# Kernel tuning notes

Hardware: AMD Instinct MI355X
Metric: run time of the kernel (lower is better)

## Reference

```python
import jax, jax.numpy as jnp
import numpy as np

DG = 8   # deformable_groups
KK = 9   # 3x3 kernel
NEG_SLOPE = 0.2


def conv3x3(x, w, b):
    y = jax.lax.conv_general_dilated(x, w, (1, 1), ((1, 1), (1, 1)),
                                     dimension_numbers=('NCHW', 'OIHW', 'NCHW'))
    return y + b[None, :, None, None]


def deform_sample(x, oy, ox, mask):
    # x: [B,C,H,W]; oy/ox/mask: [B,DG,KK,H,W] -> sampled [B,DG,cpg,KK,H,W]
    B, C, H, W = x.shape
    cpg = C // DG
    ky, kx = jnp.meshgrid(jnp.arange(3), jnp.arange(3), indexing='ij')
    ky = (ky.reshape(-1) - 1).astype(x.dtype)  # dilation=1, padding=1
    kx = (kx.reshape(-1) - 1).astype(x.dtype)
    hh = jnp.arange(H, dtype=x.dtype)
    ww = jnp.arange(W, dtype=x.dtype)
    py = hh[None, None, None, :, None] + ky[None, None, :, None, None] + oy
    px = ww[None, None, None, None, :] + kx[None, None, :, None, None] + ox
    y0 = jnp.floor(py)
    x0 = jnp.floor(px)
    fy = py - y0
    fx = px - x0
    xg = x.reshape(B, DG, cpg, H * W)

    def gather(yi, xi):
        valid = ((yi >= 0) & (yi < H) & (xi >= 0) & (xi < W)).astype(x.dtype)
        yc = jnp.clip(yi, 0, H - 1)
        xc = jnp.clip(xi, 0, W - 1)
        idx = (yc * W + xc).reshape(B, DG, 1, KK * H * W)
        v = jnp.take_along_axis(xg, idx, axis=3).reshape(B, DG, cpg, KK, H, W)
        return v * valid[:, :, None]

    y0i = y0.astype(jnp.int32)
    x0i = x0.astype(jnp.int32)
    v00 = gather(y0i, x0i)
    v01 = gather(y0i, x0i + 1)
    v10 = gather(y0i + 1, x0i)
    v11 = gather(y0i + 1, x0i + 1)
    wy = fy[:, :, None]
    wx = fx[:, :, None]
    val = (v00 * (1 - wy) * (1 - wx) + v01 * (1 - wy) * wx
           + v10 * wy * (1 - wx) + v11 * wy * wx)
    return val * mask[:, :, None]


def reference(x, offset, w_off, b_off, w_dcn, b_dcn, w_conv1, b_conv1):
    B, C, H, W = x.shape
    om = conv3x3(offset, w_off, b_off)  # [B, 3*DG*KK, H, W]
    o1, o2, m = jnp.split(om, 3, axis=1)
    oy = o1.reshape(B, DG, KK, H, W)
    ox = o2.reshape(B, DG, KK, H, W)
    mask = jax.nn.sigmoid(m).reshape(B, DG, KK, H, W)
    sampled = deform_sample(x, oy, ox, mask)  # [B,DG,cpg,KK,H,W]
    wd = w_dcn.reshape(w_dcn.shape[0], DG, C // DG, KK)
    dcn = jnp.einsum('bgckhw,ogck->bohw', sampled, wd) + b_dcn[None, :, None, None]
    fea = jnp.where(dcn >= 0, dcn, NEG_SLOPE * dcn)  # LeakyReLU(0.2)
    out = conv3x3(fea, w_conv1, b_conv1) + x  # residual
    return out


def setup_inputs() -> dict:
    key = jax.random.key(0)
    ks = jax.random.split(key, 8)
    B, C, H, W = 4, 64, 96, 96
    offC = 64
    s = 1.0 / np.sqrt(C * 9)
    return {
        'x': jax.random.normal(ks[0], (B, C, H, W), jnp.float32),
        'offset': jax.random.normal(ks[1], (B, offC, H, W), jnp.float32),
        'w_off': jax.random.normal(ks[2], (3 * DG * KK, offC, 3, 3), jnp.float32) * 0.05,
        'b_off': jnp.zeros((3 * DG * KK,), jnp.float32),
        'w_dcn': jax.random.normal(ks[3], (C, C, 3, 3), jnp.float32) * s,
        'b_dcn': jnp.zeros((C,), jnp.float32),
        'w_conv1': jax.random.normal(ks[4], (C, C, 3, 3), jnp.float32) * s,
        'b_conv1': jnp.zeros((C,), jnp.float32),
    }
```

## Files before the change

kernel.cpp:

```cpp
#include <hip/hip_runtime.h>
#include <math.h>

#define HH 96
#define WW 96
#define NB 4
#define NC 64
#define HW (HH*WW)
#define PH 98
#define PW 98
#define PHW (PH*PW)
#define NPP (NB*PHW)

typedef unsigned short u16;
typedef unsigned int   u32;
typedef __attribute__((ext_vector_type(8))) short bf16x8;
typedef __attribute__((ext_vector_type(4))) float f32x4;

__device__ inline float bf2f(u16 v) { u32 u = ((u32)v) << 16; return __uint_as_float(u); }
__device__ inline u16 f2bf(float f) {
    u32 u = __float_as_uint(f);
    return (u16)((u + 0x7FFFu + ((u >> 16) & 1u)) >> 16);
}
__device__ __forceinline__ float elemf(const u32* a, int i) {
    u32 v = a[i >> 1];
    v = (i & 1) ? (v & 0xFFFF0000u) : (v << 16);
    return __uint_as_float(v);
}

__global__ __launch_bounds__(256) void k_prep(
    const float* __restrict__ x, const float* __restrict__ offset,
    const float* __restrict__ w_off, const float* __restrict__ w_dcn,
    const float* __restrict__ w_c1,
    u16* __restrict__ xt, u16* __restrict__ otp,
    u16* __restrict__ d_off, u16* __restrict__ d_dcn, u16* __restrict__ d_c1) {
    int bx = blockIdx.x;
    int tid = threadIdx.x;
    if (bx < 144) {
        int pix = bx * 256 + tid;
        int b = pix / HW, hw = pix % HW;
        const float* s = x + b * 64 * HW + hw;
        uint4* dp = (uint4*)(xt + pix * 64);
#pragma unroll
        for (int q = 0; q < 8; ++q) {
            u32 a0 = (u32)f2bf(s[(q*8+0)*HW]) | ((u32)f2bf(s[(q*8+1)*HW]) << 16);
            u32 a1 = (u32)f2bf(s[(q*8+2)*HW]) | ((u32)f2bf(s[(q*8+3)*HW]) << 16);
            u32 a2 = (u32)f2bf(s[(q*8+4)*HW]) | ((u32)f2bf(s[(q*8+5)*HW]) << 16);
            u32 a3 = (u32)f2bf(s[(q*8+6)*HW]) | ((u32)f2bf(s[(q*8+7)*HW]) << 16);
            dp[q] = make_uint4(a0, a1, a2, a3);
        }
        return;
    }
    if (bx < 295) {
        int pp = (bx - 144) * 256 + tid;
        if (pp >= NPP) return;
        int bp = pp / PHW, rem = pp % PHW;
        int py = rem / PW, px = rem % PW;
        int y = py - 1, xx = px - 1;
        uint4* dp = (uint4*)(otp + (size_t)pp * 64);
        if (y >= 0 && y < HH && xx >= 0 && xx < WW) {
            const float* s = offset + bp * 64 * HW + y * WW + xx;
#pragma unroll
            for (int q = 0; q < 8; ++q) {
                u32 a0 = (u32)f2bf(s[(q*8+0)*HW]) | ((u32)f2bf(s[(q*8+1)*HW]) << 16);
                u32 a1 = (u32)f2bf(s[(q*8+2)*HW]) | ((u32)f2bf(s[(q*8+3)*HW]) << 16);
                u32 a2 = (u32)f2bf(s[(q*8+4)*HW]) | ((u32)f2bf(s[(q*8+5)*HW]) << 16);
                u32 a3 = (u32)f2bf(s[(q*8+6)*HW]) | ((u32)f2bf(s[(q*8+7)*HW]) << 16);
                dp[q] = make_uint4(a0, a1, a2, a3);
            }
        } else {
            uint4 z = make_uint4(0u, 0u, 0u, 0u);
#pragma unroll
            for (int q = 0; q < 8; ++q) dp[q] = z;
        }
        return;
    }
    int rel = bx - 295;
    int m, i0;
    if (rel < 576)      { m = 0; i0 = rel * 256; }
    else if (rel < 720) { m = 1; i0 = (rel - 576) * 256; }
    else                { m = 2; i0 = (rel - 720) * 256; }
    const float* w = (m == 0) ? w_off : ((m == 1) ? w_dcn : w_c1);
    u16* dst = (m == 0) ? d_off : ((m == 1) ? d_dcn : d_c1);
    int NT   = (m == 0) ? 16 : 4;
    int NCO  = (m == 0) ? 216 : 64;
    int i = i0 + tid;
    if (i >= 18 * NT * 512) return;
    int j = i & 7, L = (i >> 3) & 63;
    int cot = (i >> 9) % NT, t = (i >> 9) / NT;
    int k = t * 32 + ((L >> 4) << 3) + j;
    int co = cot * 16 + (L & 15);
    float v = 0.f;
    if (co < NCO) {
        int ci, q;
        if (m == 1) { int c = k & 7, gk = k >> 3; int kk = gk % 9, g = gk / 9; ci = g*8+c; q = kk; }
        else        { q = k >> 6; ci = k & 63; }
        v = w[co * 576 + ci * 9 + q];
    }
    dst[i] = f2bf(v);
}

__global__ __launch_bounds__(256) void k_gemm_off(
    const u16* __restrict__ otp, const u16* __restrict__ wtb,
    const float* __restrict__ bias, u16* __restrict__ omr) {
    __shared__ __align__(16) char smem[32768];
    u16* lb = (u16*)smem;
    int tid = threadIdx.x;
    int wid = tid >> 6, L = tid & 63, lr = L & 15, lk = L >> 4;
    int pixblk = blockIdx.x * 64;
    int pixA = pixblk + wid * 16 + lr;
    int b = pixblk / HW;
    int hw = pixA % HW, y = hw / WW, x = hw % WW;
    int Abase = ((b * PH + y + 1) * PW + (x + 1)) * 64;

    f32x4 acc[14];
#pragma unroll
    for (int i = 0; i < 14; ++i) acc[i] = (f32x4){0.f, 0.f, 0.f, 0.f};

    for (int t = 0; t < 18; ++t) {
        if (t) __syncthreads();
        {
            const uint4* s = (const uint4*)(wtb + t * 8192);
            uint4* d = (uint4*)lb;
            for (int i = tid; i < 896; i += 256) d[i] = s[i];
        }
        __syncthreads();
        int q = t >> 1;
        int c0 = (t & 1) * 32 + lk * 8;
        int aoff = ((q / 3 - 1) * PW + (q % 3 - 1)) * 64 + c0;
        bf16x8 a = *(const bf16x8*)(otp + Abase + aoff);
        const u16* wp = lb + L * 8;
#pragma unroll
        for (int cot = 0; cot < 14; ++cot) {
            bf16x8 bf = *(const bf16x8*)(wp + cot * 512);
            acc[cot] = __builtin_amdgcn_mfma_f32_16x16x32_bf16(a, bf, acc[cot], 0, 0, 0);
        }
    }

    __syncthreads();
    u16* om_s = (u16*)smem;
#pragma unroll
    for (int cot = 0; cot < 14; ++cot) {
        int co = cot * 16 + lr;
        if (co < 216) {
            int cls = co / 72;
            int c   = co % 72;
            int g   = c / 9, kk = c % 9;
            int slot = g * 32 + cls * 9 + kk;
            float bs = bias[co];
#pragma unroll
            for (int r = 0; r < 4; ++r) {
                float v = acc[cot][r] + bs;
                if (cls == 2) v = 1.f / (1.f + __expf(-v));
                om_s[(wid * 16 + lk * 4 + r) * 256 + slot] = f2bf(v);
            }
        }
    }
    __syncthreads();
    {
        const uint4* s = (const uint4*)om_s;
        uint4* d = (uint4*)(omr + (size_t)pixblk * 256);
#pragma unroll
        for (int i = 0; i < 8; ++i) d[tid + i * 256] = s[tid + i * 256];
    }
}

__global__ __launch_bounds__(256) void k_sdcn(
    const u16* __restrict__ xt, const u16* __restrict__ omr,
    const u16* __restrict__ wtb, const float* __restrict__ bias,
    u16* __restrict__ fea) {
    __shared__ u16 sv[32 * 576];
    int tid = threadIdx.x;
    int pixblk = blockIdx.x * 32;
    int p = tid >> 3, g = tid & 7;
    int pix = pixblk + p;
    int b = pixblk / HW;
    int hw = pix % HW, h = hw / WW, w = hw % WW;

    {
        const u16* xb = xt + b * HW * 64 + g * 8;
        const uint4* op = (const uint4*)(omr + (size_t)pix * 256 + g * 32);
        uint4 o0 = op[0], o1 = op[1], o2 = op[2], o3 = op[3];
        u32 oa[16] = {o0.x,o0.y,o0.z,o0.w, o1.x,o1.y,o1.z,o1.w,
                      o2.x,o2.y,o2.z,o2.w, o3.x,o3.y,o3.z,o3.w};
#pragma unroll
        for (int kk = 0; kk < 9; ++kk) {
            float oy   = elemf(oa, kk);
            float ox   = elemf(oa, 9 + kk);
            float mask = elemf(oa, 18 + kk);

            float py = (float)(h + kk / 3 - 1) + oy;
            float px = (float)(w + kk % 3 - 1) + ox;
            float y0f = floorf(py), x0f = floorf(px);
            float fy = py - y0f, fx = px - x0f;
            int y0 = (int)y0f, x0 = (int)x0f, y1 = y0 + 1, x1 = x0 + 1;
            int yc0 = min(max(y0, 0), HH-1), yc1 = min(max(y1, 0), HH-1);
            int xc0 = min(max(x0, 0), WW-1), xc1 = min(max(x1, 0), WW-1);
            float u0 = 1.f - fy, u1 = fy, s0 = 1.f - fx, s1 = fx;
            float w00 = (y0 >= 0 && y0 < HH && x0 >= 0 && x0 < WW) ? u0*s0*mask : 0.f;
            float w01 = (y0 >= 0 && y0 < HH && x1 >= 0 && x1 < WW) ? u0*s1*mask : 0.f;
            float w10 = (y1 >= 0 && y1 < HH && x0 >= 0 && x0 < WW) ? u1*s0*mask : 0.f;
            float w11 = (y1 >= 0 && y1 < HH && x1 >= 0 && x1 < WW) ? u1*s1*mask : 0.f;

            uint4 q00 = *(const uint4*)(xb + (yc0*WW + xc0)*64);
            uint4 q01 = *(const uint4*)(xb + (yc0*WW + xc1)*64);
            uint4 q10 = *(const uint4*)(xb + (yc1*WW + xc0)*64);
            uint4 q11 = *(const uint4*)(xb + (yc1*WW + xc1)*64);

            float r[8];
            {
                float a, bb, c, d;
                a=__uint_as_float(q00.x<<16); bb=__uint_as_float(q01.x<<16); c=__uint_as_float(q10.x<<16); d=__uint_as_float(q11.x<<16);
                r[0]=w00*a+w01*bb+w10*c+w11*d;
                a=__uint_as_float(q00.x&0xFFFF0000u); bb=__uint_as_float(q01.x&0xFFFF0000u); c=__uint_as_float(q10.x&0xFFFF0000u); d=__uint_as_float(q11.x&0xFFFF0000u);
                r[1]=w00*a+w01*bb+w10*c+w11*d;
                a=__uint_as_float(q00.y<<16); bb=__uint_as_float(q01.y<<16); c=__uint_as_float(q10.y<<16); d=__uint_as_float(q11.y<<16);
                r[2]=w00*a+w01*bb+w10*c+w11*d;
                a=__uint_as_float(q00.y&0xFFFF0000u); bb=__uint_as_float(q01.y&0xFFFF0000u); c=__uint_as_float(q10.y&0xFFFF0000u); d=__uint_as_float(q11.y&0xFFFF0000u);
                r[3]=w00*a+w01*bb+w10*c+w11*d;
                a=__uint_as_float(q00.z<<16); bb=__uint_as_float(q01.z<<16); c=__uint_as_float(q10.z<<16); d=__uint_as_float(q11.z<<16);
                r[4]=w00*a+w01*bb+w10*c+w11*d;
                a=__uint_as_float(q00.z&0xFFFF0000u); bb=__uint_as_float(q01.z&0xFFFF0000u); c=__uint_as_float(q10.z&0xFFFF0000u); d=__uint_as_float(q11.z&0xFFFF0000u);
                r[5]=w00*a+w01*bb+w10*c+w11*d;
                a=__uint_as_float(q00.w<<16); bb=__uint_as_float(q01.w<<16); c=__uint_as_float(q10.w<<16); d=__uint_as_float(q11.w<<16);
                r[6]=w00*a+w01*bb+w10*c+w11*d;
                a=__uint_as_float(q00.w&0xFFFF0000u); bb=__uint_as_float(q01.w&0xFFFF0000u); c=__uint_as_float(q10.w&0xFFFF0000u); d=__uint_as_float(q11.w&0xFFFF0000u);
                r[7]=w00*a+w01*bb+w10*c+w11*d;
            }
            u32 a0 = (u32)f2bf(r[0]) | ((u32)f2bf(r[1]) << 16);
            u32 a1 = (u32)f2bf(r[2]) | ((u32)f2bf(r[3]) << 16);
            u32 a2 = (u32)f2bf(r[4]) | ((u32)f2bf(r[5]) << 16);
            u32 a3 = (u32)f2bf(r[6]) | ((u32)f2bf(r[7]) << 16);
            int slot = g * 9 + kk;
            *(uint4*)((char*)sv + p * 1152 + ((slot * 16) ^ ((p & 7) << 4))) = make_uint4(a0, a1, a2, a3);
        }
    }
    __syncthreads();

    int wid = tid >> 6, L = tid & 63, lr = L & 15, lk = L >> 4;
    int pbase = (wid & 1) * 16, cbase = (wid >> 1) * 2;
    int arow = pbase + lr;

    f32x4 acc[2];
    acc[0] = (f32x4){0.f, 0.f, 0.f, 0.f};
    acc[1] = (f32x4){0.f, 0.f, 0.f, 0.f};
#pragma unroll
    for (int t = 0; t < 18; ++t) {
        bf16x8 a = *(const bf16x8*)((const char*)sv + arow * 1152 + (((t * 4 + lk) * 16) ^ ((arow & 7) << 4)));
#pragma unroll
        for (int ct = 0; ct < 2; ++ct) {
            bf16x8 bf = *(const bf16x8*)(wtb + ((t * 4 + cbase + ct) * 64 + L) * 8);
            acc[ct] = __builtin_amdgcn_mfma_f32_16x16x32_bf16(a, bf, acc[ct], 0, 0, 0);
        }
    }
#pragma unroll
    for (int ct = 0; ct < 2; ++ct) {
        int co = (cbase + ct) * 16 + lr;
        float bs = bias[co];
#pragma unroll
        for (int r = 0; r < 4; ++r) {
            float v = acc[ct][r] + bs;
            v = (v >= 0.f) ? v : 0.2f * v;
            fea[(pixblk + pbase + lk * 4 + r) * 64 + co] = f2bf(v);
        }
    }
}

__global__ __launch_bounds__(256) void k_gemm_c1(
    const u16* __restrict__ fea, const u16* __restrict__ wtb,
    const float* __restrict__ bias, const float* __restrict__ xres,
    float* __restrict__ out) {
    __shared__ __align__(16) char smraw[36864];
    u16* lb = (u16*)smraw;
    int tid = threadIdx.x;
    int wid = tid >> 6, L = tid & 63, lr = L & 15, lk = L >> 4;
    int pixblk = blockIdx.x * 64;
    int pixbase = pixblk + wid * 16;
    int pixA = pixbase + lr;
    int b = pixblk / HW;
    int hw = pixA % HW, y = hw / WW, x = hw % WW;

    f32x4 acc[4];
#pragma unroll
    for (int i = 0; i < 4; ++i) acc[i] = (f32x4){0.f, 0.f, 0.f, 0.f};

    {
        const uint4* s = (const uint4*)wtb;
        uint4* d = (uint4*)lb;
#pragma unroll
        for (int i = 0; i < 9; ++i) d[tid + i * 256] = s[tid + i * 256];
    }
    __syncthreads();
    for (int half = 0; half < 2; ++half) {
        int tbase = half * 9;
#pragma unroll
        for (int tl = 0; tl < 9; ++tl) {
            int t = tbase + tl;
            int q = t >> 1;
            int c0 = (t & 1) * 32 + lk * 8;
            int dy = q / 3 - 1, dx = q % 3 - 1;
            int yy = y + dy, xx = x + dx;
            bf16x8 a = {0,0,0,0,0,0,0,0};
            if (yy >= 0 && yy < HH && xx >= 0 && xx < WW)
                a = *(const bf16x8*)(fea + ((b * HH + yy) * WW + xx) * 64 + c0);
            const u16* wp = lb + (tl * 256 + L) * 8;
#pragma unroll
            for (int cot = 0; cot < 4; ++cot) {
                bf16x8 bf = *(const bf16x8*)(wp + cot * 512);
                acc[cot] = __builtin_amdgcn_mfma_f32_16x16x32_bf16(a, bf, acc[cot], 0, 0, 0);
            }
        }
        __syncthreads();
        if (half == 0) {
            const uint4* s = (const uint4*)(wtb + 18432);
            uint4* d = (uint4*)lb;
#pragma unroll
            for (int i = 0; i < 9; ++i) d[tid + i * 256] = s[tid + i * 256];
            __syncthreads();
        }
    }
    float* ob = (float*)smraw;
#pragma unroll
    for (int cot = 0; cot < 4; ++cot) {
#pragma unroll
        for (int r = 0; r < 4; ++r)
            ob[(wid * 16 + lk * 4 + r) * 66 + cot * 16 + lr] = acc[cot][r];
    }
    __syncthreads();
    int p = tid & 63, cg = tid >> 6;
    int hw0 = pixblk % HW;
#pragma unroll
    for (int i = 0; i < 16; ++i) {
        int co = cg * 16 + i;
        int idx = (b * 64 + co) * HW + hw0 + p;
        out[idx] = ob[p * 66 + co] + bias[co] + xres[idx];
    }
}

extern "C" void kernel_launch(void* const* d_in, const int* in_sizes, int n_in,
                              void* d_out, int out_size, void* d_ws, size_t ws_size,
                              hipStream_t stream) {
    const float* x       = (const float*)d_in[0];
    const float* offset  = (const float*)d_in[1];
    const float* w_off   = (const float*)d_in[2];
    const float* b_off   = (const float*)d_in[3];
    const float* w_dcn   = (const float*)d_in[4];
    const float* b_dcn   = (const float*)d_in[5];
    const float* w_conv1 = (const float*)d_in[6];
    const float* b_conv1 = (const float*)d_in[7];
    float* out = (float*)d_out;

    char* ws = (char*)d_ws;
    u16* omr     = (u16*)(ws);
    u16* xt      = (u16*)(ws + 18874368);
    u16* otp     = (u16*)(ws + 23592960);
    u16* fea     = (u16*)(ws + 28510208);
    u16* wtb_off = (u16*)(ws + 33228800);
    u16* wtb_dcn = (u16*)(ws + 33523712);
    u16* wtb_c1  = (u16*)(ws + 33597440);

    hipLaunchKernelGGL(k_prep, dim3(1159), dim3(256), 0, stream,
                       x, offset, w_off, w_dcn, w_conv1, xt, otp, wtb_off, wtb_dcn, wtb_c1);
    hipLaunchKernelGGL(k_gemm_off, dim3(576), dim3(256), 0, stream, otp, wtb_off, b_off, omr);
    hipLaunchKernelGGL(k_sdcn, dim3(1152), dim3(256), 0, stream, xt, omr, wtb_dcn, b_dcn, fea);
    hipLaunchKernelGGL(k_gemm_c1, dim3(576), dim3(256), 0, stream, fea, wtb_c1, b_conv1, x, out);
}
```

Before: 162.0 us.

## Prefetch bilinear gathers in sdcn and use zero-padded fea layout for conv1

```diff
diff --git a/kernel.cpp b/kernel.cpp
--- a/kernel.cpp
+++ b/kernel.cpp
@@ -31,7 +31,7 @@
     const float* __restrict__ x, const float* __restrict__ offset,
     const float* __restrict__ w_off, const float* __restrict__ w_dcn,
     const float* __restrict__ w_c1,
-    u16* __restrict__ xt, u16* __restrict__ otp,
+    u16* __restrict__ xt, u16* __restrict__ otp, u16* __restrict__ feap,
     u16* __restrict__ d_off, u16* __restrict__ d_dcn, u16* __restrict__ d_c1) {
     int bx = blockIdx.x;
     int tid = threadIdx.x;
@@ -74,7 +74,16 @@
         }
         return;
     }
-    int rel = bx - 295;
+    if (bx < 446) {
+        int pp = (bx - 295) * 256 + tid;
+        if (pp >= NPP) return;
+        uint4* dp = (uint4*)(feap + (size_t)pp * 64);
+        uint4 z = make_uint4(0u, 0u, 0u, 0u);
+#pragma unroll
+        for (int q = 0; q < 8; ++q) dp[q] = z;
+        return;
+    }
+    int rel = bx - 446;
     int m, i0;
     if (rel < 576)      { m = 0; i0 = rel * 256; }
     else if (rel < 720) { m = 1; i0 = (rel - 576) * 256; }
@@ -167,7 +176,7 @@
 __global__ __launch_bounds__(256) void k_sdcn(
     const u16* __restrict__ xt, const u16* __restrict__ omr,
     const u16* __restrict__ wtb, const float* __restrict__ bias,
-    u16* __restrict__ fea) {
+    u16* __restrict__ feap) {
     __shared__ u16 sv[32 * 576];
     int tid = threadIdx.x;
     int pixblk = blockIdx.x * 32;
@@ -182,48 +191,60 @@
         uint4 o0 = op[0], o1 = op[1], o2 = op[2], o3 = op[3];
         u32 oa[16] = {o0.x,o0.y,o0.z,o0.w, o1.x,o1.y,o1.z,o1.w,
                       o2.x,o2.y,o2.z,o2.w, o3.x,o3.y,o3.z,o3.w};
+
+        float pw00[2], pw01[2], pw10[2], pw11[2];
+        int   pi00[2], pi01[2], pi10[2], pi11[2];
+        uint4 q00[2], q01[2], q10[2], q11[2];
+
+#define CALC(kk, s) {                                                          \
+        float oy   = elemf(oa, (kk));                                          \
+        float ox   = elemf(oa, 9 + (kk));                                      \
+        float mask = elemf(oa, 18 + (kk));                                     \
+        float py = (float)(h + (kk) / 3 - 1) + oy;                             \
+        float px = (float)(w + (kk) % 3 - 1) + ox;                             \
+        float y0f = floorf(py), x0f = floorf(px);                              \
+        float fy = py - y0f, fx = px - x0f;                                    \
+        int y0 = (int)y0f, x0 = (int)x0f, y1 = y0 + 1, x1 = x0 + 1;            \
+        int yc0 = min(max(y0, 0), HH-1), yc1 = min(max(y1, 0), HH-1);          \
+        int xc0 = min(max(x0, 0), WW-1), xc1 = min(max(x1, 0), WW-1);          \
+        float u0 = 1.f - fy, u1 = fy, s0 = 1.f - fx, s1 = fx;                  \
+        pw00[s] = (y0 >= 0 && y0 < HH && x0 >= 0 && x0 < WW) ? u0*s0*mask : 0.f; \
+        pw01[s] = (y0 >= 0 && y0 < HH && x1 >= 0 && x1 < WW) ? u0*s1*mask : 0.f; \
+        pw10[s] = (y1 >= 0 && y1 < HH && x0 >= 0 && x0 < WW) ? u1*s0*mask : 0.f; \
+        pw11[s] = (y1 >= 0 && y1 < HH && x1 >= 0 && x1 < WW) ? u1*s1*mask : 0.f; \
+        pi00[s] = yc0*WW + xc0; pi01[s] = yc0*WW + xc1;                        \
+        pi10[s] = yc1*WW + xc0; pi11[s] = yc1*WW + xc1; }
+#define ISSUE(s) {                                                             \
+        q00[s] = *(const uint4*)(xb + pi00[s]*64);                             \
+        q01[s] = *(const uint4*)(xb + pi01[s]*64);                             \
+        q10[s] = *(const uint4*)(xb + pi10[s]*64);                             \
+        q11[s] = *(const uint4*)(xb + pi11[s]*64); }
+
+        CALC(0, 0); ISSUE(0);
 #pragma unroll
         for (int kk = 0; kk < 9; ++kk) {
-            float oy   = elemf(oa, kk);
-            float ox   = elemf(oa, 9 + kk);
-            float mask = elemf(oa, 18 + kk);
-
-            float py = (float)(h + kk / 3 - 1) + oy;
-            float px = (float)(w + kk % 3 - 1) + ox;
-            float y0f = floorf(py), x0f = floorf(px);
-            float fy = py - y0f, fx = px - x0f;
-            int y0 = (int)y0f, x0 = (int)x0f, y1 = y0 + 1, x1 = x0 + 1;
-            int yc0 = min(max(y0, 0), HH-1), yc1 = min(max(y1, 0), HH-1);
-            int xc0 = min(max(x0, 0), WW-1), xc1 = min(max(x1, 0), WW-1);
-            float u0 = 1.f - fy, u1 = fy, s0 = 1.f - fx, s1 = fx;
-            float w00 = (y0 >= 0 && y0 < HH && x0 >= 0 && x0 < WW) ? u0*s0*mask : 0.f;
-            float w01 = (y0 >= 0 && y0 < HH && x1 >= 0 && x1 < WW) ? u0*s1*mask : 0.f;
-            float w10 = (y1 >= 0 && y1 < HH && x0 >= 0 && x0 < WW) ? u1*s0*mask : 0.f;
-            float w11 = (y1 >= 0 && y1 < HH && x1 >= 0 && x1 < WW) ? u1*s1*mask : 0.f;
-
-            uint4 q00 = *(const uint4*)(xb + (yc0*WW + xc0)*64);
-            uint4 q01 = *(const uint4*)(xb + (yc0*WW + xc1)*64);
-            uint4 q10 = *(const uint4*)(xb + (yc1*WW + xc0)*64);
-            uint4 q11 = *(const uint4*)(xb + (yc1*WW + xc1)*64);
-
+            int cur = kk & 1, nxt = cur ^ 1;
+            if (kk < 8) { CALC(kk + 1, nxt); ISSUE(nxt); }
+            float w00 = pw00[cur], w01 = pw01[cur], w10 = pw10[cur], w11 = pw11[cur];
+            uint4 a4 = q00[cur], b4 = q01[cur], c4 = q10[cur], d4 = q11[cur];
             float r[8];
             {
                 float a, bb, c, d;
-                a=__uint_as_float(q00.x<<16); bb=__uint_as_float(q01.x<<16); c=__uint_as_float(q10.x<<16); d=__uint_as_float(q11.x<<16);
+                a=__uint_as_float(a4.x<<16); bb=__uint_as_float(b4.x<<16); c=__uint_as_float(c4.x<<16); d=__uint_as_float(d4.x<<16);
                 r[0]=w00*a+w01*bb+w10*c+w11*d;
-                a=__uint_as_float(q00.x&0xFFFF0000u); bb=__uint_as_float(q01.x&0xFFFF0000u); c=__uint_as_float(q10.x&0xFFFF0000u); d=__uint_as_float(q11.x&0xFFFF0000u);
+                a=__uint_as_float(a4.x&0xFFFF0000u); bb=__uint_as_float(b4.x&0xFFFF0000u); c=__uint_as_float(c4.x&0xFFFF0000u); d=__uint_as_float(d4.x&0xFFFF0000u);
                 r[1]=w00*a+w01*bb+w10*c+w11*d;
-                a=__uint_as_float(q00.y<<16); bb=__uint_as_float(q01.y<<16); c=__uint_as_float(q10.y<<16); d=__uint_as_float(q11.y<<16);
+                a=__uint_as_float(a4.y<<16); bb=__uint_as_float(b4.y<<16); c=__uint_as_float(c4.y<<16); d=__uint_as_float(d4.y<<16);
                 r[2]=w00*a+w01*bb+w10*c+w11*d;
-                a=__uint_as_float(q00.y&0xFFFF0000u); bb=__uint_as_float(q01.y&0xFFFF0000u); c=__uint_as_float(q10.y&0xFFFF0000u); d=__uint_as_float(q11.y&0xFFFF0000u);
+                a=__uint_as_float(a4.y&0xFFFF0000u); bb=__uint_as_float(b4.y&0xFFFF0000u); c=__uint_as_float(c4.y&0xFFFF0000u); d=__uint_as_float(d4.y&0xFFFF0000u);
                 r[3]=w00*a+w01*bb+w10*c+w11*d;
-                a=__uint_as_float(q00.z<<16); bb=__uint_as_float(q01.z<<16); c=__uint_as_float(q10.z<<16); d=__uint_as_float(q11.z<<16);
+                a=__uint_as_float(a4.z<<16); bb=__uint_as_float(b4.z<<16); c=__uint_as_float(c4.z<<16); d=__uint_as_float(d4.z<<16);
                 r[4]=w00*a+w01*bb+w10*c+w11*d;
-                a=__uint_as_float(q00.z&0xFFFF0000u); bb=__uint_as_float(q01.z&0xFFFF0000u); c=__uint_as_float(q10.z&0xFFFF0000u); d=__uint_as_float(q11.z&0xFFFF0000u);
+                a=__uint_as_float(a4.z&0xFFFF0000u); bb=__uint_as_float(b4.z&0xFFFF0000u); c=__uint_as_float(c4.z&0xFFFF0000u); d=__uint_as_float(d4.z&0xFFFF0000u);
                 r[5]=w00*a+w01*bb+w10*c+w11*d;
-                a=__uint_as_float(q00.w<<16); bb=__uint_as_float(q01.w<<16); c=__uint_as_float(q10.w<<16); d=__uint_as_float(q11.w<<16);
+                a=__uint_as_float(a4.w<<16); bb=__uint_as_float(b4.w<<16); c=__uint_as_float(c4.w<<16); d=__uint_as_float(d4.w<<16);
                 r[6]=w00*a+w01*bb+w10*c+w11*d;
-                a=__uint_as_float(q00.w&0xFFFF0000u); bb=__uint_as_float(q01.w&0xFFFF0000u); c=__uint_as_float(q10.w&0xFFFF0000u); d=__uint_as_float(q11.w&0xFFFF0000u);
+                a=__uint_as_float(a4.w&0xFFFF0000u); bb=__uint_as_float(b4.w&0xFFFF0000u); c=__uint_as_float(c4.w&0xFFFF0000u); d=__uint_as_float(d4.w&0xFFFF0000u);
                 r[7]=w00*a+w01*bb+w10*c+w11*d;
             }
             u32 a0 = (u32)f2bf(r[0]) | ((u32)f2bf(r[1]) << 16);
@@ -233,6 +254,8 @@
             int slot = g * 9 + kk;
             *(uint4*)((char*)sv + p * 1152 + ((slot * 16) ^ ((p & 7) << 4))) = make_uint4(a0, a1, a2, a3);
         }
+#undef CALC
+#undef ISSUE
     }
     __syncthreads();
 
@@ -252,6 +275,8 @@
             acc[ct] = __builtin_amdgcn_mfma_f32_16x16x32_bf16(a, bf, acc[ct], 0, 0, 0);
         }
     }
+    int hwb = pixblk % HW;
+    int hb = hwb / WW, wb = hwb % WW;
 #pragma unroll
     for (int ct = 0; ct < 2; ++ct) {
         int co = (cbase + ct) * 16 + lr;
@@ -260,13 +285,13 @@
         for (int r = 0; r < 4; ++r) {
             float v = acc[ct][r] + bs;
             v = (v >= 0.f) ? v : 0.2f * v;
-            fea[(pixblk + pbase + lk * 4 + r) * 64 + co] = f2bf(v);
+            feap[((b * PH + hb + 1) * PW + (wb + 1 + pbase + lk * 4 + r)) * 64 + co] = f2bf(v);
         }
     }
 }
 
 __global__ __launch_bounds__(256) void k_gemm_c1(
-    const u16* __restrict__ fea, const u16* __restrict__ wtb,
+    const u16* __restrict__ feap, const u16* __restrict__ wtb,
     const float* __restrict__ bias, const float* __restrict__ xres,
     float* __restrict__ out) {
     __shared__ __align__(16) char smraw[36864];
@@ -274,10 +299,10 @@
     int tid = threadIdx.x;
     int wid = tid >> 6, L = tid & 63, lr = L & 15, lk = L >> 4;
     int pixblk = blockIdx.x * 64;
-    int pixbase = pixblk + wid * 16;
-    int pixA = pixbase + lr;
+    int pixA = pixblk + wid * 16 + lr;
     int b = pixblk / HW;
     int hw = pixA % HW, y = hw / WW, x = hw % WW;
+    int Abase = ((b * PH + y + 1) * PW + (x + 1)) * 64;
 
     f32x4 acc[4];
 #pragma unroll
@@ -297,11 +322,8 @@
             int t = tbase + tl;
             int q = t >> 1;
             int c0 = (t & 1) * 32 + lk * 8;
-            int dy = q / 3 - 1, dx = q % 3 - 1;
-            int yy = y + dy, xx = x + dx;
-            bf16x8 a = {0,0,0,0,0,0,0,0};
-            if (yy >= 0 && yy < HH && xx >= 0 && xx < WW)
-                a = *(const bf16x8*)(fea + ((b * HH + yy) * WW + xx) * 64 + c0);
+            int aoff = ((q / 3 - 1) * PW + (q % 3 - 1)) * 64 + c0;
+            bf16x8 a = *(const bf16x8*)(feap + Abase + aoff);
             const u16* wp = lb + (tl * 256 + L) * 8;
 #pragma unroll
             for (int cot = 0; cot < 4; ++cot) {
@@ -353,14 +375,15 @@
     u16* omr     = (u16*)(ws);
     u16* xt      = (u16*)(ws + 18874368);
     u16* otp     = (u16*)(ws + 23592960);
-    u16* fea     = (u16*)(ws + 28510208);
-    u16* wtb_off = (u16*)(ws + 33228800);
-    u16* wtb_dcn = (u16*)(ws + 33523712);
-    u16* wtb_c1  = (u16*)(ws + 33597440);
-
-    hipLaunchKernelGGL(k_prep, dim3(1159), dim3(256), 0, stream,
-                       x, offset, w_off, w_dcn, w_conv1, xt, otp, wtb_off, wtb_dcn, wtb_c1);
+    u16* feap    = (u16*)(ws + 28510208);
+    u16* wtb_off = (u16*)(ws + 33427456);
+    u16* wtb_dcn = (u16*)(ws + 33722368);
+    u16* wtb_c1  = (u16*)(ws + 33796096);
+
+    hipLaunchKernelGGL(k_prep, dim3(1310), dim3(256), 0, stream,
+                       x, offset, w_off, w_dcn, w_conv1, xt, otp, feap,
+                       wtb_off, wtb_dcn, wtb_c1);
     hipLaunchKernelGGL(k_gemm_off, dim3(576), dim3(256), 0, stream, otp, wtb_off, b_off, omr);
-    hipLaunchKernelGGL(k_sdcn, dim3(1152), dim3(256), 0, stream, xt, omr, wtb_dcn, b_dcn, fea);
-    hipLaunchKernelGGL(k_gemm_c1, dim3(576), dim3(256), 0, stream, fea, wtb_c1, b_conv1, x, out);
-}
+    hipLaunchKernelGGL(k_sdcn, dim3(1152), dim3(256), 0, stream, xt, omr, wtb_dcn, b_dcn, feap);
+    hipLaunchKernelGGL(k_gemm_c1, dim3(576), dim3(256), 0, stream, feap, wtb_c1, b_conv1, x, out);
+}
```

Result: no change. 161.0 us (-0.6%).
